# Performance work log

Measured on AMD Instinct MI355X. Metric: run time of the kernel, lower is better.

Reference implementation:

```python
import jax, jax.numpy as jnp
import numpy as np

EMBED_DIM = 1024
NUM_HEADS = 16
HEAD_DIM = EMBED_DIM // NUM_HEADS


def setup_inputs() -> dict:
    key = jax.random.key(0)
    k_x, k_wqkv, k_bqkv, k_wout, k_bout = jax.random.split(key, 5)
    s = 1.0 / np.sqrt(EMBED_DIM)
    return {
        "x": jax.random.normal(k_x, (2, 2048, EMBED_DIM), dtype=jnp.float32),
        "w_qkv": jax.random.uniform(k_wqkv, (EMBED_DIM, 3 * EMBED_DIM), jnp.float32, -s, s),
        "b_qkv": jax.random.uniform(k_bqkv, (3 * EMBED_DIM,), jnp.float32, -s, s),
        "w_out": jax.random.uniform(k_wout, (EMBED_DIM, EMBED_DIM), jnp.float32, -s, s),
        "b_out": jax.random.uniform(k_bout, (EMBED_DIM,), jnp.float32, -s, s),
    }


def reference(x, w_qkv, b_qkv, w_out, b_out):
    B, S, D = x.shape
    H, Hd = NUM_HEADS, HEAD_DIM
    # qkv projection, then per-head chunk: layout matches torch view(B,S,H,3*Hd).chunk(3,-1)
    qkv = (x @ w_qkv + b_qkv).reshape(B, S, H, 3, Hd)  # [B,S,H,3,Hd]
    q = qkv[..., 0, :]  # [B,S,H,Hd]
    k = qkv[..., 1, :]
    v = qkv[..., 2, :]
    scale = 1.0 / np.sqrt(Hd).astype(np.float32)
    scores = jnp.einsum("bqhd,bkhd->bhqk", q, k) * scale  # [B,H,S,S]
    probs = jax.nn.softmax(scores, axis=-1)
    out = jnp.einsum("bhqk,bkhd->bqhd", probs, v).reshape(B, S, D)
    return out @ w_out + b_out
```

## Files before the change

kernel.cpp:

```cpp
#include <hip/hip_runtime.h>
#include <hip/hip_bf16.h>


typedef __bf16 bf16;
typedef __bf16 bf16x8 __attribute__((ext_vector_type(8)));
typedef float  f32x4  __attribute__((ext_vector_type(4)));
typedef float  f32x16 __attribute__((ext_vector_type(16)));
typedef unsigned int uint;
typedef unsigned int uint2v __attribute__((ext_vector_type(2)));

__device__ __forceinline__ void gload_lds16(const void* g, void* l) {
  __builtin_amdgcn_global_load_lds(
      (const __attribute__((address_space(1))) unsigned int*)g,
      (__attribute__((address_space(3))) unsigned int*)l, 16, 0, 0);
}

__device__ __forceinline__ uint pkbf16(float lo, float hi) {
  union { bf16 h[2]; uint u; } t;
  t.h[0] = (bf16)lo; t.h[1] = (bf16)hi;
  return t.u;
}

__device__ __forceinline__ void pl32swapu(uint& a, uint& b) {
  uint2v r = __builtin_amdgcn_permlane32_swap(a, b, false, false);
  a = r.x; b = r.y;
}
__device__ __forceinline__ void pl32swapf(float& a, float& b) {
  uint ua = __builtin_bit_cast(uint, a), ub = __builtin_bit_cast(uint, b);
  pl32swapu(ua, ub);
  a = __builtin_bit_cast(float, ua); b = __builtin_bit_cast(float, ub);
}

__global__ __launch_bounds__(256) void k_convert(const float* __restrict__ in,
                                                 bf16* __restrict__ out, int n) {
  int i = (blockIdx.x * blockDim.x + threadIdx.x) * 8;
  if (i >= n) return;
  float4 a = *(const float4*)(in + i);
  float4 b = *(const float4*)(in + i + 4);
  bf16x8 o;
  o[0] = (bf16)a.x; o[1] = (bf16)a.y; o[2] = (bf16)a.z; o[3] = (bf16)a.w;
  o[4] = (bf16)b.x; o[5] = (bf16)b.y; o[6] = (bf16)b.z; o[7] = (bf16)b.w;
  *(bf16x8*)(out + i) = o;
}

template<bool PERM>
__global__ __launch_bounds__(256) void k_transpose(const float* __restrict__ in,
                                                   bf16* __restrict__ out, int K, int N) {
  __shared__ float tile[32][33];
  int n0 = blockIdx.x * 32, k0 = blockIdx.y * 32;
  int tx = threadIdx.x, ty = threadIdx.y;
#pragma unroll
  for (int i = 0; i < 4; i++)
    tile[ty + i * 8][tx] = in[(size_t)(k0 + ty + i * 8) * N + n0 + tx];
  __syncthreads();
#pragma unroll
  for (int i = 0; i < 4; i++) {
    int n = n0 + ty + i * 8;
    int row = n;
    if (PERM) {
      int rem = n % 192;
      row = (rem >> 6) * 1024 + (n / 192) * 64 + (rem & 63);
    }
    out[(size_t)row * K + k0 + tx] = (bf16)tile[tx][ty + i * 8];
  }
}

template<int BM, int BN>
__device__ __forceinline__ void gemm_tile(const bf16* __restrict__ A, const bf16* __restrict__ B,
                                          int K, int m0, int n0,
                                          bf16* As, bf16* Bs, f32x4 acc[BM / 32][BN / 32]) {
  const int tid  = threadIdx.x;
  const int lane = tid & 63;
  const int wr   = (tid >> 7) & 1;
  const int wc   = (tid >> 6) & 1;
  constexpr int LA = BM / 64, LB = BN / 64;
  auto stage = [&](int k0, int b) {
#pragma unroll
    for (int i = 0; i < LA; i++) {
      int row = i * 64 + (tid >> 2);
      int sw  = (tid & 3) ^ (row & 3);
      gload_lds16(A + (size_t)(m0 + row) * K + k0 + sw * 8, (char*)As + b * (BM * 64) + i * 4096 + tid * 16);
    }
#pragma unroll
    for (int i = 0; i < LB; i++) {
      int row = i * 64 + (tid >> 2);
      int sw  = (tid & 3) ^ (row & 3);
      gload_lds16(B + (size_t)(n0 + row) * K + k0 + sw * 8, (char*)Bs + b * (BN * 64) + i * 4096 + tid * 16);
    }
  };
  const int nk = K / 32;
  stage(0, 0); stage(32, 1); stage(64, 2);
  for (int t = 0; t < nk; t++) {
    if (t < nk - 2) {
      if constexpr (LA + LB == 4) asm volatile("s_waitcnt vmcnt(8)" ::: "memory");
      else                        asm volatile("s_waitcnt vmcnt(6)" ::: "memory");
    } else if (t < nk - 1) {
      if constexpr (LA + LB == 4) asm volatile("s_waitcnt vmcnt(4)" ::: "memory");
      else                        asm volatile("s_waitcnt vmcnt(3)" ::: "memory");
    } else {
      asm volatile("s_waitcnt vmcnt(0)" ::: "memory");
    }
    __builtin_amdgcn_s_barrier();
    asm volatile("" ::: "memory");
    if (t + 3 < nk) stage((t + 3) * 32, (t + 3) & 3);
    const int cur = t & 3;
    bf16x8 af[BM / 32], bfr[BN / 32];
#pragma unroll
    for (int r = 0; r < BM / 32; r++) {
      int ra = wr * (BM / 2) + r * 16 + (lane & 15);
      af[r]  = *(const bf16x8*)((const char*)As + cur * (BM * 64) + ra * 64 + ((((lane >> 4) << 4)) ^ ((ra & 3) << 4)));
    }
#pragma unroll
    for (int c = 0; c < BN / 32; c++) {
      int rb = wc * (BN / 2) + c * 16 + (lane & 15);
      bfr[c] = *(const bf16x8*)((const char*)Bs + cur * (BN * 64) + rb * 64 + ((((lane >> 4) << 4)) ^ ((rb & 3) << 4)));
    }
#pragma unroll
    for (int r = 0; r < BM / 32; r++)
#pragma unroll
      for (int c = 0; c < BN / 32; c++)
        acc[r][c] = __builtin_amdgcn_mfma_f32_16x16x32_bf16(af[r], bfr[c], acc[r][c], 0, 0, 0);
    asm volatile("" ::: "memory");
  }
}

__global__ __launch_bounds__(256) void k_gemm_qkv(const bf16* __restrict__ A, const bf16* __restrict__ Bt,
                                                  const float* __restrict__ bias,
                                                  bf16* __restrict__ qb, bf16* __restrict__ kb,
                                                  bf16* __restrict__ vtb) {
  __shared__ char GS[65536];
  bf16* As = (bf16*)GS;
  bf16* Bs = (bf16*)(GS + 32768);
  int m0 = blockIdx.x * 128, n0 = blockIdx.y * 128;
  f32x4 zero = {0.f, 0.f, 0.f, 0.f};
  f32x4 acc[4][4];
#pragma unroll
  for (int r = 0; r < 4; r++)
#pragma unroll
    for (int c = 0; c < 4; c++) acc[r][c] = zero;
  gemm_tile<128, 128>(A, Bt, 1024, m0, n0, As, Bs, acc);

  const int tid  = threadIdx.x;
  const int lane = tid & 63;
  const int wr = (tid >> 7) & 1, wc = (tid >> 6) & 1;
  const int group = n0 >> 10;
  const int hb = (n0 & 1023) >> 6;
  const int b_ = m0 >> 11;
  const float QSs = 0.125f * 1.4426950408889634f;

  __syncthreads();
  char* TL = GS;
#pragma unroll
  for (int r = 0; r < 4; r++) {
    int mloc = wr * 64 + r * 16 + ((lane >> 4) << 2);
#pragma unroll
    for (int c = 0; c < 4; c++) {
      int nloc = wc * 64 + c * 16 + (lane & 15);
      int np = n0 + nloc;
      float bv = bias[((np & 1023) >> 6) * 192 + group * 64 + (np & 63)];
#pragma unroll
      for (int g = 0; g < 4; g++) {
        float v = acc[r][c][g] + bv;
        if (group == 0) v *= QSs;
        int row = (group < 2) ? (mloc + g) : nloc;
        int col = (group < 2) ? nloc : (mloc + g);
        *(bf16*)(TL + row * 256 + col * 2) = (bf16)v;
      }
    }
  }
  __syncthreads();
  if (group < 2) {
    bf16* dst = (group == 0) ? qb : kb;
#pragma unroll
    for (int it = 0; it < 8; it++) {
      int cid = it * 256 + tid;
      int sl = cid >> 4, sub = cid & 15;
      int hh = hb + (sub >> 3), ck = sub & 7;
      bf16x8 v8 = *(const bf16x8*)(TL + sl * 256 + (sub << 4));
      *(bf16x8*)(dst + ((size_t)(b_ * 16 + hh) * 2048 + (m0 & 2047) + sl) * 64 + ck * 8) = v8;
    }
  } else {
#pragma unroll
    for (int it = 0; it < 8; it++) {
      int cid = it * 256 + tid;
      int row = cid >> 4, ck = cid & 15;
      int hh = hb + (row >> 6), dd = row & 63;
      bf16x8 v8 = *(const bf16x8*)(TL + row * 256 + (ck << 4));
      *(bf16x8*)(vtb + ((size_t)(b_ * 16 + hh) * 64 + dd) * 2048 + (m0 & 2047) + ck * 8) = v8;
    }
  }
}

__global__ __launch_bounds__(256) void k_gemm_out(const bf16* __restrict__ A, const bf16* __restrict__ Bt,
                                                  const float* __restrict__ bias,
                                                  float* __restrict__ out) {
  __shared__ bf16 As[4 * 64 * 32];
  __shared__ bf16 Bs[4 * 128 * 32];
  int m0 = blockIdx.x * 64, n0 = blockIdx.y * 128;
  f32x4 zero = {0.f, 0.f, 0.f, 0.f};
  f32x4 acc[2][4];
#pragma unroll
  for (int r = 0; r < 2; r++)
#pragma unroll
    for (int c = 0; c < 4; c++) acc[r][c] = zero;
  gemm_tile<64, 128>(A, Bt, 1024, m0, n0, As, Bs, acc);
  const int lane = threadIdx.x & 63;
  const int wr = (threadIdx.x >> 7) & 1, wc = (threadIdx.x >> 6) & 1;
#pragma unroll
  for (int r = 0; r < 2; r++) {
    int mbase = m0 + wr * 32 + r * 16 + ((lane >> 4) << 2);
#pragma unroll
    for (int c = 0; c < 4; c++) {
      int n = n0 + wc * 64 + c * 16 + (lane & 15);
      float bv = bias[n];
#pragma unroll
      for (int g = 0; g < 4; g++)
        out[(size_t)(mbase + g) * 1024 + n] = acc[r][c][g] + bv;
    }
  }
}

__global__ __launch_bounds__(512, 4) void k_attn(const bf16* __restrict__ qb, const bf16* __restrict__ kb,
                                                 const bf16* __restrict__ vtb, bf16* __restrict__ ob) {
  __shared__ char SMEM[73728];
  const int tid  = threadIdx.x;
  const int lane = tid & 63;
  const int wave = tid >> 6;
  const int qsub = wave & 3;
  const int half = wave >> 2;
  const int ln31 = lane & 31;
  const int g    = lane >> 5;

  int l = blockIdx.x;
  int x = l & 7, j = l >> 3;
  int qt = j & 15;
  int bh = x * 4 + (j >> 4);

  const int q0 = qt * 128 + qsub * 32;

  bf16x8 qf[4];
  {
    const bf16* qp = qb + ((size_t)bh * 2048 + q0 + ln31) * 64 + g * 8;
#pragma unroll
    for (int dc = 0; dc < 4; dc++) qf[dc] = *(const bf16x8*)(qp + dc * 16);
  }

  const f32x16 z16 = 0.f;
  f32x16 O0 = 0.f, O1 = 0.f;
  float lacc[4] = {0.f, 0.f, 0.f, 0.f};
  bf16x8 pf[4];

  const int c1 = tid, r1 = c1 / 9, cc1 = c1 % 9;
  const int of1 = (cc1 == 8 ? 0 : cc1) * 8;
  const int c2 = 512 + tid, r2 = c2 / 9, cc2 = c2 % 9;
  const int of2 = (cc2 == 8 ? 0 : cc2) * 8;
  const bf16* kg0a = kb  + ((size_t)bh * 2048 +        r1) * 64 + of1;
  const bf16* kg1a = kb  + ((size_t)bh * 2048 + 1024 + r1) * 64 + of1;
  const bf16* vg0a = vtb + ((size_t)bh * 64 + r1) * 2048 +        of1;
  const bf16* vg1a = vtb + ((size_t)bh * 64 + r1) * 2048 + 1024 + of1;
  const bf16* kg0b = kb  + ((size_t)bh * 2048 +        r2) * 64 + of2;
  const bf16* kg1b = kb  + ((size_t)bh * 2048 + 1024 + r2) * 64 + of2;
  const bf16* vg0b = vtb + ((size_t)bh * 64 + r2) * 2048 +        of2;
  const bf16* vg1b = vtb + ((size_t)bh * 64 + r2) * 2048 + 1024 + of2;
  auto stage = [&](int t, int s) {
    char* bs = SMEM + s * 36864;
    gload_lds16(kg0a + (size_t)t * 4096, bs +         c1 * 16);
    gload_lds16(kg1a + (size_t)t * 4096, bs + 9216  + c1 * 16);
    gload_lds16(vg0a + t * 64,           bs + 18432 + c1 * 16);
    gload_lds16(vg1a + t * 64,           bs + 27648 + c1 * 16);
    if (wave == 0) {
      gload_lds16(kg0b + (size_t)t * 4096, bs +         c2 * 16);
      gload_lds16(kg1b + (size_t)t * 4096, bs + 9216  + c2 * 16);
      gload_lds16(vg0b + t * 64,           bs + 18432 + c2 * 16);
      gload_lds16(vg1b + t * 64,           bs + 27648 + c2 * 16);
    }
  };

  stage(0, 0);
  for (int t = 0; t < 16; t++) {
    asm volatile("s_waitcnt vmcnt(0)" ::: "memory");
    __builtin_amdgcn_s_barrier();
    asm volatile("" ::: "memory");
    if (t + 1 < 16) stage(t + 1, (t + 1) & 1);

    const char* Kc = SMEM + (t & 1) * 36864 + half * 9216;
    const char* Vc = SMEM + (t & 1) * 36864 + 18432 + half * 9216;
    const char* kr0 = Kc + ln31 * 144;
    const char* kr1 = Kc + (32 + ln31) * 144;

    f32x16 s0v, s1v;
    __builtin_amdgcn_s_setprio(1);
    {
      bf16x8 k0 = *(const bf16x8*)(kr0 + (g << 4));
      bf16x8 k1 = *(const bf16x8*)(kr1 + (g << 4));
      s0v = __builtin_amdgcn_mfma_f32_32x32x16_bf16(k0, qf[0], z16, 0, 0, 0);
      s1v = __builtin_amdgcn_mfma_f32_32x32x16_bf16(k1, qf[0], z16, 0, 0, 0);
    }
#pragma unroll
    for (int dc = 1; dc < 4; dc++) {
      bf16x8 ka = *(const bf16x8*)(kr0 + ((dc * 2 + g) << 4));
      bf16x8 kb_ = *(const bf16x8*)(kr1 + ((dc * 2 + g) << 4));
      s0v = __builtin_amdgcn_mfma_f32_32x32x16_bf16(ka, qf[dc], s0v, 0, 0, 0);
      s1v = __builtin_amdgcn_mfma_f32_32x32x16_bf16(kb_, qf[dc], s1v, 0, 0, 0);
    }
    __builtin_amdgcn_s_setprio(0);

#pragma unroll
    for (int r = 0; r < 16; r++) {
      s0v[r] = __builtin_amdgcn_exp2f(s0v[r]);
      s1v[r] = __builtin_amdgcn_exp2f(s1v[r]);
    }
#pragma unroll
    for (int r = 0; r < 4; r++)
      lacc[r] += ((s0v[r] + s0v[r + 4]) + (s0v[r + 8] + s0v[r + 12]))
               + ((s1v[r] + s1v[r + 4]) + (s1v[r + 8] + s1v[r + 12]));
#pragma unroll
    for (int kc = 0; kc < 4; kc++) {
      const int rb = (kc & 1) * 8;
      uint w0, w1, w2, w3;
      if (kc < 2) {
        w0 = pkbf16(s0v[rb + 0], s0v[rb + 1]); w1 = pkbf16(s0v[rb + 2], s0v[rb + 3]);
        w2 = pkbf16(s0v[rb + 4], s0v[rb + 5]); w3 = pkbf16(s0v[rb + 6], s0v[rb + 7]);
      } else {
        w0 = pkbf16(s1v[rb + 0], s1v[rb + 1]); w1 = pkbf16(s1v[rb + 2], s1v[rb + 3]);
        w2 = pkbf16(s1v[rb + 4], s1v[rb + 5]); w3 = pkbf16(s1v[rb + 6], s1v[rb + 7]);
      }
      pl32swapu(w0, w2);
      pl32swapu(w1, w3);
      union { uint w[4]; bf16x8 v; } pu;
      pu.w[0] = w0; pu.w[1] = w1; pu.w[2] = w2; pu.w[3] = w3;
      pf[kc] = pu.v;
    }

    __builtin_amdgcn_s_setprio(1);
#pragma unroll
    for (int kc = 0; kc < 4; kc++) {
      bf16x8 vf0 = *(const bf16x8*)(Vc + ln31 * 144 + ((kc * 2 + g) << 4));
      bf16x8 vf1 = *(const bf16x8*)(Vc + (32 + ln31) * 144 + ((kc * 2 + g) << 4));
      O0 = __builtin_amdgcn_mfma_f32_32x32x16_bf16(vf0, pf[kc], O0, 0, 0, 0);
      O1 = __builtin_amdgcn_mfma_f32_32x32x16_bf16(vf1, pf[kc], O1, 0, 0, 0);
    }
    __builtin_amdgcn_s_setprio(0);
    asm volatile("" ::: "memory");
  }

  float l_r = (lacc[0] + lacc[1]) + (lacc[2] + lacc[3]);
  { float o = l_r; pl32swapf(l_r, o); l_r += o; }

  float* Opart = (float*)SMEM;
  float* Ls    = (float*)(SMEM + 36864);
  __syncthreads();
  if (half == 1) {
    float* my = Opart + (qsub * 64 + lane) * 36;
#pragma unroll
    for (int c = 0; c < 4; c++) {
      f32x4 a = {O0[c * 4], O0[c * 4 + 1], O0[c * 4 + 2], O0[c * 4 + 3]};
      f32x4 b = {O1[c * 4], O1[c * 4 + 1], O1[c * 4 + 2], O1[c * 4 + 3]};
      *(f32x4*)(my + c * 4) = a;
      *(f32x4*)(my + 16 + c * 4) = b;
    }
    if (lane < 32) Ls[qsub * 32 + ln31] = l_r;
  }
  __syncthreads();
  bf16 (*Os)[32][72] = reinterpret_cast<bf16 (*)[32][72]>(SMEM + 40960);
  if (half == 0) {
    const float* pr = Opart + (qsub * 64 + lane) * 36;
#pragma unroll
    for (int c = 0; c < 4; c++) {
      f32x4 a = *(const f32x4*)(pr + c * 4);
      f32x4 b = *(const f32x4*)(pr + 16 + c * 4);
#pragma unroll
      for (int k = 0; k < 4; k++) { O0[c * 4 + k] += a[k]; O1[c * 4 + k] += b[k]; }
    }
    l_r += Ls[qsub * 32 + ln31];
    float inv = 1.0f / l_r;
#pragma unroll
    for (int r = 0; r < 16; r++) {
      int d0 = (r & 3) + 8 * (r >> 2) + 4 * g;
      Os[qsub][ln31][d0]      = (bf16)(O0[r] * inv);
      Os[qsub][ln31][d0 + 32] = (bf16)(O1[r] * inv);
    }
  }
  __syncthreads();
  if (half == 0) {
    int b_ = bh >> 4, h = bh & 15;
#pragma unroll
    for (int it = 0; it < 4; it++) {
      int cid = it * 64 + lane;
      int row = cid >> 3, c = cid & 7;
      bf16x8 v8o = *(const bf16x8*)&Os[qsub][row][c * 8];
      *(bf16x8*)(ob + ((size_t)(b_ * 2048 + q0 + row)) * 1024 + h * 64 + c * 8) = v8o;
    }
  }
}

extern "C" void kernel_launch(void* const* d_in, const int* in_sizes, int n_in,
                              void* d_out, int out_size, void* d_ws, size_t ws_size,
                              hipStream_t stream) {
  const float* x     = (const float*)d_in[0];
  const float* w_qkv = (const float*)d_in[1];
  const float* b_qkv = (const float*)d_in[2];
  const float* w_out = (const float*)d_in[3];
  const float* b_out = (const float*)d_in[4];
  float* out = (float*)d_out;

  char* ws = (char*)d_ws;
  bf16* xb  = (bf16*)ws;
  bf16* wqT = (bf16*)(ws + (8ull  << 20));
  bf16* woT = (bf16*)(ws + (14ull << 20));
  bf16* qb  = (bf16*)(ws + (16ull << 20));
  bf16* kb  = (bf16*)(ws + (24ull << 20));
  bf16* vtb = (bf16*)(ws + (32ull << 20));

  k_convert<<<2048, 256, 0, stream>>>(x, xb, 4194304);
  k_transpose<true><<<dim3(96, 32), dim3(32, 8), 0, stream>>>(w_qkv, wqT, 1024, 3072);
  k_transpose<false><<<dim3(32, 32), dim3(32, 8), 0, stream>>>(w_out, woT, 1024, 1024);
  k_gemm_qkv<<<dim3(32, 24), 256, 0, stream>>>(xb, wqT, b_qkv, qb, kb, vtb);
  k_attn<<<512, 512, 0, stream>>>(qb, kb, vtb, xb);
  k_gemm_out<<<dim3(64, 8), 256, 0, stream>>>(xb, woT, b_out, out);
}
```

Before: 122.7 us.

## Enlarge QKV GEMM tile to 256x256 with 8 waves and double-buffered LDS

The QKV projection GEMM moves from 128x128 tiles with 4 waves to 256x256 tiles with 8 waves. It uses a custom double-buffered global-to-LDS pipeline with BK=64, XOR-swizzled LDS layout, and s_setprio around the MFMA block. The epilogue is rewritten to use a swizzled 512-byte-row staging buffer in the 128KB LDS. The aim is more data reuse per block and better latency hiding. In exchange the grid shrinks to 192 blocks, which may underfill the 256 CUs, and register and LDS pressure rises.

```diff
diff --git a/kernel.cpp b/kernel.cpp
--- a/kernel.cpp
+++ b/kernel.cpp
@@ -124,69 +124,146 @@
   }
 }
 
-__global__ __launch_bounds__(256) void k_gemm_qkv(const bf16* __restrict__ A, const bf16* __restrict__ Bt,
-                                                  const float* __restrict__ bias,
-                                                  bf16* __restrict__ qb, bf16* __restrict__ kb,
-                                                  bf16* __restrict__ vtb) {
-  __shared__ char GS[65536];
-  bf16* As = (bf16*)GS;
-  bf16* Bs = (bf16*)(GS + 32768);
-  int m0 = blockIdx.x * 128, n0 = blockIdx.y * 128;
-  f32x4 zero = {0.f, 0.f, 0.f, 0.f};
-  f32x4 acc[4][4];
-#pragma unroll
-  for (int r = 0; r < 4; r++)
-#pragma unroll
-    for (int c = 0; c < 4; c++) acc[r][c] = zero;
-  gemm_tile<128, 128>(A, Bt, 1024, m0, n0, As, Bs, acc);
-
+__global__ __launch_bounds__(512, 2) void k_gemm_qkv(const bf16* __restrict__ A, const bf16* __restrict__ Bt,
+                                                     const float* __restrict__ bias,
+                                                     bf16* __restrict__ qb, bf16* __restrict__ kb,
+                                                     bf16* __restrict__ vtb) {
+  __shared__ char GS[131072];
   const int tid  = threadIdx.x;
   const int lane = tid & 63;
-  const int wr = (tid >> 7) & 1, wc = (tid >> 6) & 1;
+  const int wave = tid >> 6;
+  const int wr   = wave >> 2;
+  const int wc   = wave & 3;
+  const int m0 = blockIdx.x * 256, n0 = blockIdx.y * 256;
+  const int K = 1024;
+
+  f32x4 acc[8][4];
+  f32x4 zero = {0.f, 0.f, 0.f, 0.f};
+#pragma unroll
+  for (int ms = 0; ms < 8; ms++)
+#pragma unroll
+    for (int ns = 0; ns < 4; ns++) acc[ms][ns] = zero;
+
+  auto stage = [&](int t, int b) {
+    int k0 = t * 64;
+#pragma unroll
+    for (int i = 0; i < 4; i++) {
+      int cid = i * 512 + tid;
+      int row = cid >> 3, c = cid & 7;
+      gload_lds16(A + (size_t)(m0 + row) * K + k0 + ((c ^ (row & 7)) * 8),
+                  GS + b * 32768 + cid * 16);
+    }
+#pragma unroll
+    for (int i = 0; i < 4; i++) {
+      int cid = i * 512 + tid;
+      int row = cid >> 3, c = cid & 7;
+      gload_lds16(Bt + (size_t)(n0 + row) * K + k0 + ((c ^ (row & 7)) * 8),
+                  GS + 65536 + b * 32768 + cid * 16);
+    }
+  };
+
+  stage(0, 0);
+  for (int t = 0; t < 16; t++) {
+    const int b = t & 1;
+    if (t + 1 < 16) {
+      stage(t + 1, b ^ 1);
+      asm volatile("s_waitcnt vmcnt(8)" ::: "memory");
+    } else {
+      asm volatile("s_waitcnt vmcnt(0)" ::: "memory");
+    }
+    __builtin_amdgcn_s_barrier();
+    asm volatile("" ::: "memory");
+    const char* Ab = GS + b * 32768;
+    const char* Bb = GS + 65536 + b * 32768;
+#pragma unroll
+    for (int ks = 0; ks < 2; ks++) {
+      bf16x8 af[8], bf_[4];
+#pragma unroll
+      for (int ms = 0; ms < 8; ms++) {
+        int row = wr * 128 + ms * 16 + (lane & 15);
+        int ch = (ks * 4 + (lane >> 4)) ^ (row & 7);
+        af[ms] = *(const bf16x8*)(Ab + row * 128 + ch * 16);
+      }
+#pragma unroll
+      for (int ns = 0; ns < 4; ns++) {
+        int row = wc * 64 + ns * 16 + (lane & 15);
+        int ch = (ks * 4 + (lane >> 4)) ^ (row & 7);
+        bf_[ns] = *(const bf16x8*)(Bb + row * 128 + ch * 16);
+      }
+      __builtin_amdgcn_s_setprio(1);
+#pragma unroll
+      for (int ms = 0; ms < 8; ms++)
+#pragma unroll
+        for (int ns = 0; ns < 4; ns++)
+          acc[ms][ns] = __builtin_amdgcn_mfma_f32_16x16x32_bf16(af[ms], bf_[ns], acc[ms][ns], 0, 0, 0);
+      __builtin_amdgcn_s_setprio(0);
+    }
+    asm volatile("" ::: "memory");
+    __builtin_amdgcn_s_barrier();
+    asm volatile("" ::: "memory");
+  }
+
   const int group = n0 >> 10;
   const int hb = (n0 & 1023) >> 6;
   const int b_ = m0 >> 11;
   const float QSs = 0.125f * 1.4426950408889634f;
-
-  __syncthreads();
   char* TL = GS;
-#pragma unroll
-  for (int r = 0; r < 4; r++) {
-    int mloc = wr * 64 + r * 16 + ((lane >> 4) << 2);
-#pragma unroll
-    for (int c = 0; c < 4; c++) {
-      int nloc = wc * 64 + c * 16 + (lane & 15);
-      int np = n0 + nloc;
-      float bv = bias[((np & 1023) >> 6) * 192 + group * 64 + (np & 63)];
-#pragma unroll
-      for (int g = 0; g < 4; g++) {
-        float v = acc[r][c][g] + bv;
-        if (group == 0) v *= QSs;
-        int row = (group < 2) ? (mloc + g) : nloc;
-        int col = (group < 2) ? nloc : (mloc + g);
-        *(bf16*)(TL + row * 256 + col * 2) = (bf16)v;
+
+  if (group < 2) {
+#pragma unroll
+    for (int ms = 0; ms < 8; ms++) {
+      int mloc = wr * 128 + ms * 16 + ((lane >> 4) << 2);
+#pragma unroll
+      for (int ns = 0; ns < 4; ns++) {
+        int nloc = wc * 64 + ns * 16 + (lane & 15);
+        int np = n0 + nloc;
+        float bv = bias[((np & 1023) >> 6) * 192 + group * 64 + (np & 63)];
+#pragma unroll
+        for (int g = 0; g < 4; g++) {
+          float v = acc[ms][ns][g] + bv;
+          if (group == 0) v *= QSs;
+          int m = mloc + g;
+          int byte = m * 512 + ((((nloc >> 3) ^ (m & 7)) << 4) | ((nloc & 7) << 1));
+          *(bf16*)(TL + byte) = (bf16)v;
+        }
       }
     }
-  }
-  __syncthreads();
-  if (group < 2) {
+    __syncthreads();
     bf16* dst = (group == 0) ? qb : kb;
 #pragma unroll
-    for (int it = 0; it < 8; it++) {
-      int cid = it * 256 + tid;
-      int sl = cid >> 4, sub = cid & 15;
-      int hh = hb + (sub >> 3), ck = sub & 7;
-      bf16x8 v8 = *(const bf16x8*)(TL + sl * 256 + (sub << 4));
-      *(bf16x8*)(dst + ((size_t)(b_ * 16 + hh) * 2048 + (m0 & 2047) + sl) * 64 + ck * 8) = v8;
+    for (int it = 0; it < 16; it++) {
+      int cid = it * 512 + tid;
+      int row = cid >> 5, cc = cid & 31;
+      int hh = hb + (cc >> 3), ck = cc & 7;
+      bf16x8 v8 = *(const bf16x8*)(TL + row * 512 + ((cc ^ (row & 7)) << 4));
+      *(bf16x8*)(dst + ((size_t)(b_ * 16 + hh) * 2048 + (m0 & 2047) + row) * 64 + ck * 8) = v8;
     }
   } else {
 #pragma unroll
-    for (int it = 0; it < 8; it++) {
-      int cid = it * 256 + tid;
-      int row = cid >> 4, ck = cid & 15;
+    for (int ms = 0; ms < 8; ms++) {
+      int mloc = wr * 128 + ms * 16 + ((lane >> 4) << 2);
+#pragma unroll
+      for (int ns = 0; ns < 4; ns++) {
+        int nloc = wc * 64 + ns * 16 + (lane & 15);
+        int np = n0 + nloc;
+        float bv = bias[((np & 1023) >> 6) * 192 + 2 * 64 + (np & 63)];
+#pragma unroll
+        for (int g = 0; g < 4; g++) {
+          float v = acc[ms][ns][g] + bv;
+          int m = mloc + g;
+          int byte = nloc * 512 + ((((m >> 3) ^ (nloc & 7)) << 4) | ((m & 7) << 1));
+          *(bf16*)(TL + byte) = (bf16)v;
+        }
+      }
+    }
+    __syncthreads();
+#pragma unroll
+    for (int it = 0; it < 16; it++) {
+      int cid = it * 512 + tid;
+      int row = cid >> 5, mc = cid & 31;
       int hh = hb + (row >> 6), dd = row & 63;
-      bf16x8 v8 = *(const bf16x8*)(TL + row * 256 + (ck << 4));
-      *(bf16x8*)(vtb + ((size_t)(b_ * 16 + hh) * 64 + dd) * 2048 + (m0 & 2047) + ck * 8) = v8;
+      bf16x8 v8 = *(const bf16x8*)(TL + row * 512 + ((mc ^ (row & 7)) << 4));
+      *(bf16x8*)(vtb + ((size_t)(b_ * 16 + hh) * 64 + dd) * 2048 + (m0 & 2047) + mc * 8) = v8;
     }
   }
 }
@@ -415,7 +492,7 @@
   k_convert<<<2048, 256, 0, stream>>>(x, xb, 4194304);
   k_transpose<true><<<dim3(96, 32), dim3(32, 8), 0, stream>>>(w_qkv, wqT, 1024, 3072);
   k_transpose<false><<<dim3(32, 32), dim3(32, 8), 0, stream>>>(w_out, woT, 1024, 1024);
-  k_gemm_qkv<<<dim3(32, 24), 256, 0, stream>>>(xb, wqT, b_qkv, qb, kb, vtb);
+  k_gemm_qkv<<<dim3(16, 12), 512, 0, stream>>>(xb, wqT, b_qkv, qb, kb, vtb);
   k_attn<<<512, 512, 0, stream>>>(qb, kb, vtb, xb);
   k_gemm_out<<<dim3(64, 8), 256, 0, stream>>>(xb, woT, b_out, out);
 }
```

Result: faster. 117.5 us (-4.2%).
